# Optimization experiments

Measured on AMD Instinct MI355X. Metric: run time of the kernel, lower is better.

The kernel has to match this reference:

```python
import jax, jax.numpy as jnp
import numpy as np

W, B, C, H = 1600, 4, 1, 900
DENSITY = 0.03          # fraction of valid radar returns per column
DEPTH_MAX = 80.0        # metric depth range


def setup_inputs() -> dict:
    key = jax.random.key(0)
    k1, k2, k3 = jax.random.split(key, 3)
    radar_depth = jax.random.uniform(k1, (W, B, C, H, 1), jnp.float32) * DEPTH_MAX + 1.0
    radar_mask = jax.random.uniform(k2, (W, B, C, H, 1), jnp.float32) < DENSITY
    radar_patches = jnp.where(radar_mask, radar_depth, 0.0)
    # dense monocular depth estimate, strictly positive (all 'valid')
    mde_out_patches = jax.random.uniform(k3, (W, B, C, H, 1), jnp.float32) * DEPTH_MAX + 1.0
    return {"radar_patches": radar_patches, "mde_out_patches": mde_out_patches}


def _process_column(radar_col, mde_col):
    """Sequentially place valid radar depths of one (w,b) column.

    radar_col, mde_col: [H] float (channel 0 of the column).
    Returns radar_gt column [H].
    Matches torch loop: for each valid radar y (ascending), pick mde row with
    closest depth (argmin |mde - d|, first index on ties); if that slot is
    already occupied, search outward offsets +1,-1,+2,-2,... for an empty slot;
    if none found, overwrite the best slot.
    """
    h = radar_col.shape[0]
    ys = jnp.arange(h)
    mde_valid = mde_col != 0
    has_mde = jnp.any(mde_valid)
    BIG = jnp.float32(1e30)
    KBIG = 4 * h  # sentinel key for occupied slots

    def step(col, y):
        depth = radar_col[y]
        valid = depth != 0
        # per-point argmin over valid mde depths
        diffs = jnp.where(mde_valid, jnp.abs(mde_col - depth), BIG)
        best_y = jnp.where(has_mde, jnp.argmin(diffs), y)
        # outward collision search as a vectorized argmin over a priority key:
        #   best_y itself -> 0; offset o, +dy before -dy -> 2*o + (dy<0)
        occ = col != 0
        dy = ys - best_y
        key = 2 * jnp.abs(dy) + (dy < 0).astype(jnp.int32)
        key = jnp.where(ys == best_y, 0, key)
        key = jnp.where(occ, KBIG, key)
        final_y = jnp.argmin(key)
        # all slots occupied -> fall back to best_y (torch overwrites there)
        final_y = jnp.where(key[final_y] >= KBIG, best_y, final_y)
        new_col = jnp.where(valid, col.at[final_y].set(depth), col)
        return new_col, None

    col, _ = jax.lax.scan(step, jnp.zeros(h, radar_col.dtype), ys)
    return col


def reference(radar_patches, mde_out_patches):
    # channel 0 only is read/written, as in the torch code
    radar0 = radar_patches[:, :, 0, :, 0]   # [W, B, H]
    mde0 = mde_out_patches[:, :, 0, :, 0]   # [W, B, H]
    cols = jax.vmap(jax.vmap(_process_column))(radar0, mde0)  # [W, B, H]
    w, b, h = cols.shape
    c = radar_patches.shape[2]
    radar_gt = jnp.zeros((b, c, h, w), radar_patches.dtype)
    radar_gt = radar_gt.at[:, 0].set(jnp.transpose(cols, (1, 2, 0)))  # [B, H, W]
    return radar_gt
```

## Files before the change

### kernel.cpp

```cpp
#include <hip/hip_runtime.h>
#include <cstdint>
#include <cstddef>

#define WDIM 1600
#define BDIM 4
#define HDIM 900
#define NV4  225
#define QCAP 96
#define KBIG (4 * HDIM)
#define BW   6
#define NWAVE 4

#define DPP_MINF(v, ctrl)                                                  \
    v = fminf(v, __int_as_float(__builtin_amdgcn_update_dpp(               \
            __float_as_int(v), __float_as_int(v), ctrl, 0xf, 0xf, false)))

#define WAVE_FENCE() asm volatile("s_waitcnt lgkmcnt(0)" ::: "memory")

__global__ __launch_bounds__(256, 4) void radar_place_kernel(
    const float* __restrict__ radar, const float* __restrict__ mde,
    float* __restrict__ colout , int direct, float* __restrict__ out)
{
    __shared__ __align__(16) float s_col_all[NWAVE][HDIM];
    __shared__ float s_qd_all[NWAVE][QCAP];
    __shared__ int   s_qy_all[NWAVE][QCAP];

    const int lane = threadIdx.x & 63;
    const int wv   = threadIdx.x >> 6;
    const int colid = blockIdx.x * NWAVE + wv;

    float* s_col = s_col_all[wv];
    float* s_qd  = s_qd_all[wv];
    int*   s_qy  = s_qy_all[wv];

    const float4* mde4   = (const float4*)mde   + (long)colid * NV4;
    const float4* radar4 = (const float4*)radar + (long)colid * NV4;
    float4* col4 = (float4*)s_col;

    const unsigned long long below = (1ull << lane) - 1ull;

    bool hm = false;
#pragma unroll
    for (int c = 0; c < 4; ++c) {
        int i4 = c * 64 + lane;
        if (i4 < NV4) {
            float4 mv = mde4[i4];
            hm = hm || (mv.x != 0.f) || (mv.y != 0.f) || (mv.z != 0.f) || (mv.w != 0.f);
            col4[i4] = mv;
        }
    }
    const bool has_mde = (__ballot(hm) != 0ull);

    int Q = 0;
#pragma unroll
    for (int c = 0; c < 4; ++c) {
        int i4 = c * 64 + lane;
        bool in = (i4 < NV4);
        float4 rv = in ? radar4[i4] : make_float4(0.f, 0.f, 0.f, 0.f);
        unsigned long long b0 = __ballot(rv.x != 0.f);
        unsigned long long b1 = __ballot(rv.y != 0.f);
        unsigned long long b2 = __ballot(rv.z != 0.f);
        unsigned long long b3 = __ballot(rv.w != 0.f);
        int pos = Q + __popcll(b0 & below) + __popcll(b1 & below)
                    + __popcll(b2 & below) + __popcll(b3 & below);
        int y0 = i4 * 4;
        if (rv.x != 0.f) { if (pos < QCAP) { s_qd[pos] = rv.x; s_qy[pos] = y0;     } pos++; }
        if (rv.y != 0.f) { if (pos < QCAP) { s_qd[pos] = rv.y; s_qy[pos] = y0 + 1; } pos++; }
        if (rv.z != 0.f) { if (pos < QCAP) { s_qd[pos] = rv.z; s_qy[pos] = y0 + 2; } pos++; }
        if (rv.w != 0.f) { if (pos < QCAP) { s_qd[pos] = rv.w; s_qy[pos] = y0 + 3; } pos++; }
        Q += __popcll(b0) + __popcll(b1) + __popcll(b2) + __popcll(b3);
    }
    if (Q > QCAP) Q = QCAP;

    WAVE_FENCE();

    float m[15];
    if (lane < 60) {
        int yb = lane * 15;
#pragma unroll
        for (int k = 0; k < 15; ++k) {
            float v = s_col[yb + k];
            m[k] = (v != 0.f) ? v : 1e30f;
        }
    } else {
#pragma unroll
        for (int k = 0; k < 15; ++k) m[k] = 1e30f;
    }

    WAVE_FENCE();

#pragma unroll
    for (int c = 0; c < 4; ++c) {
        int i4 = c * 64 + lane;
        if (i4 < NV4) col4[i4] = make_float4(0.f, 0.f, 0.f, 0.f);
    }

    unsigned occ = (lane >= 60) ? 0x7FFFu : 0u;

    for (int t = 0; t < Q; t += BW) {
        float d[BW];
#pragma unroll
        for (int i = 0; i < BW; ++i) {
            int idx = (t + i < Q) ? (t + i) : (Q - 1);
            d[i] = s_qd[idx];
        }
        float bd[BW], bo[BW];
        int bik[BW];
#pragma unroll
        for (int i = 0; i < BW; ++i) { bd[i] = 3.4e38f; bik[i] = 0; }
#pragma unroll
        for (int k = 0; k < 15; ++k) {
            float mm = m[k];
#pragma unroll
            for (int i = 0; i < BW; ++i) {
                float af = fabsf(mm - d[i]);
                if (af < bd[i]) { bd[i] = af; bik[i] = k; }
            }
        }
#pragma unroll
        for (int i = 0; i < BW; ++i) bo[i] = bd[i];
#pragma unroll
        for (int i = 0; i < BW; ++i) DPP_MINF(bd[i], 0x111);
#pragma unroll
        for (int i = 0; i < BW; ++i) DPP_MINF(bd[i], 0x112);
#pragma unroll
        for (int i = 0; i < BW; ++i) DPP_MINF(bd[i], 0x114);
#pragma unroll
        for (int i = 0; i < BW; ++i) DPP_MINF(bd[i], 0x118);
#pragma unroll
        for (int i = 0; i < BW; ++i) DPP_MINF(bd[i], 0x142);
#pragma unroll
        for (int i = 0; i < BW; ++i) DPP_MINF(bd[i], 0x143);

#pragma unroll
        for (int i = 0; i < BW; ++i) {
            if (t + i < Q) {
                int best;
                if (has_mde) {
                    float gm = __int_as_float(
                        __builtin_amdgcn_readlane(__float_as_int(bd[i]), 63));
                    unsigned long long wm = __ballot(bo[i] == gm);
                    int win = __ffsll((long long)wm) - 1;
                    int kst = __shfl(bik[i], win);
                    best = win * 15 + kst;
                } else {
                    best = s_qy[t + i];
                }
                float depth = d[i];
                int sb = __builtin_amdgcn_readfirstlane(best);
                int bl = sb / 15, bk = sb % 15;
                unsigned long long bm = __ballot((occ >> bk) & 1u);
                int final_y = sb;
                if ((bm >> bl) & 1ull) {
                    int ko = 0x7fffffff, kk = 0;
#pragma unroll
                    for (int k = 0; k < 15; ++k) {
                        int yy = lane * 15 + k;
                        int o = (occ >> k) & 1;
                        int dy = yy - sb;
                        int ad = dy < 0 ? -dy : dy;
                        int key = o ? KBIG : (2 * ad + (dy < 0 ? 1 : 0));
                        if (key < ko) { ko = key; kk = k; }
                    }
                    int kmin = ko;
#pragma unroll
                    for (int off = 32; off; off >>= 1) {
                        int v = __shfl_xor(kmin, off);
                        kmin = (v < kmin) ? v : kmin;
                    }
                    if (kmin < KBIG) {
                        unsigned long long wm2 = __ballot(ko == kmin);
                        int w2 = __ffsll((long long)wm2) - 1;
                        int k2 = __shfl(kk, w2);
                        final_y = w2 * 15 + k2;
                    }
                }
                int sf = __builtin_amdgcn_readfirstlane(final_y);
                int fl = sf / 15, fk = sf % 15;
                if (lane == fl) occ |= (1u << fk);
                if (lane == 0) s_col[sf] = depth;
            }
        }
    }

    WAVE_FENCE();

    if (direct) {
        int w_ = colid >> 2, b_ = colid & 3;
#pragma unroll
        for (int c = 0; c < 4; ++c) {
            int i4 = c * 64 + lane;
            if (i4 < NV4) {
                float4 v = col4[i4];
                int y = i4 * 4;
                out[((long)(b_ * HDIM + y + 0)) * WDIM + w_] = v.x;
                out[((long)(b_ * HDIM + y + 1)) * WDIM + w_] = v.y;
                out[((long)(b_ * HDIM + y + 2)) * WDIM + w_] = v.z;
                out[((long)(b_ * HDIM + y + 3)) * WDIM + w_] = v.w;
            }
        }
    } else {
        float4* colout4 = (float4*)colout + (long)colid * NV4;
#pragma unroll
        for (int c = 0; c < 4; ++c) {
            int i4 = c * 64 + lane;
            if (i4 < NV4) colout4[i4] = col4[i4];
        }
    }
}

__global__ __launch_bounds__(256) void transpose_kernel(
    const float* __restrict__ colout, float* __restrict__ out)
{
    __shared__ float tile[32][33];
    const int b  = blockIdx.z;
    const int h0 = blockIdx.x * 32;
    const int w0 = blockIdx.y * 32;
    const int tx = threadIdx.x & 31;
    const int ty = threadIdx.x >> 5;
#pragma unroll
    for (int j = 0; j < 4; ++j) {
        int wl = ty + j * 8;
        int w = w0 + wl;
        int h = h0 + tx;
        float v = 0.0f;
        if (h < HDIM && w < WDIM) v = colout[((long)(w * BDIM + b)) * HDIM + h];
        tile[wl][tx] = v;
    }
    __syncthreads();
#pragma unroll
    for (int j = 0; j < 4; ++j) {
        int hl = ty + j * 8;
        int h = h0 + hl;
        int w = w0 + tx;
        if (h < HDIM && w < WDIM)
            out[((long)(b * HDIM + h)) * WDIM + w] = tile[tx][hl];
    }
}

extern "C" void kernel_launch(void* const* d_in, const int* in_sizes, int n_in,
                              void* d_out, int out_size, void* d_ws, size_t ws_size,
                              hipStream_t stream) {
    const float* radar = (const float*)d_in[0];
    const float* mde   = (const float*)d_in[1];
    float* out = (float*)d_out;
    float* ws  = (float*)d_ws;

    const size_t need = (size_t)WDIM * BDIM * HDIM * sizeof(float);
    const int direct = (ws_size < need) ? 1 : 0;

    hipLaunchKernelGGL(radar_place_kernel,
                       dim3(WDIM * BDIM / NWAVE), dim3(64 * NWAVE), 0, stream,
                       radar, mde, ws, direct, out);

    if (!direct) {
        dim3 g((HDIM + 31) / 32, WDIM / 32, BDIM);
        hipLaunchKernelGGL(transpose_kernel, g, dim3(256), 0, stream, ws, out);
    }
}
```

Measured before the change: 137.3 us.

## Split argmin pass from serial placement and decode collision slot from key

The per-point nearest-depth argmin now runs as a separate batched phase that writes each best row into the shared queue, with the batch width raised from 6 to 8. The serial placement loop then only resolves collisions. Queue entries are read into registers and broadcast with readlane, and the winning slot is recovered directly from the minimum priority key, so the second ballot and shuffle are gone. The integer min reduction uses DPP instead of xor shuffles. The intent is to shorten the serial dependency chain per radar point, at the cost of an extra pass and more register use.

```diff
diff --git a/kernel.cpp b/kernel.cpp
--- a/kernel.cpp
+++ b/kernel.cpp
@@ -8,12 +8,16 @@
 #define NV4  225
 #define QCAP 96
 #define KBIG (4 * HDIM)
-#define BW   6
+#define BW   8
 #define NWAVE 4
 
 #define DPP_MINF(v, ctrl)                                                  \
     v = fminf(v, __int_as_float(__builtin_amdgcn_update_dpp(               \
             __float_as_int(v), __float_as_int(v), ctrl, 0xf, 0xf, false)))
+
+#define DPP_MINI(v, ctrl)                                                  \
+    { int _dt = __builtin_amdgcn_update_dpp(v, v, ctrl, 0xf, 0xf, false);  \
+      v = (_dt < v) ? _dt : v; }
 
 #define WAVE_FENCE() asm volatile("s_waitcnt lgkmcnt(0)" ::: "memory")
 
@@ -95,92 +99,106 @@
         if (i4 < NV4) col4[i4] = make_float4(0.f, 0.f, 0.f, 0.f);
     }
 
+    if (has_mde) {
+        for (int t = 0; t < Q; t += BW) {
+            float d[BW];
+#pragma unroll
+            for (int i = 0; i < BW; ++i) {
+                int idx = (t + i < Q) ? (t + i) : (Q - 1);
+                d[i] = s_qd[idx];
+            }
+            float bd[BW], bo[BW];
+            int bik[BW];
+#pragma unroll
+            for (int i = 0; i < BW; ++i) { bd[i] = 3.4e38f; bik[i] = 0; }
+#pragma unroll
+            for (int k = 0; k < 15; ++k) {
+                float mm = m[k];
+#pragma unroll
+                for (int i = 0; i < BW; ++i) {
+                    float af = fabsf(mm - d[i]);
+                    if (af < bd[i]) { bd[i] = af; bik[i] = k; }
+                }
+            }
+#pragma unroll
+            for (int i = 0; i < BW; ++i) bo[i] = bd[i];
+#pragma unroll
+            for (int i = 0; i < BW; ++i) DPP_MINF(bd[i], 0x111);
+#pragma unroll
+            for (int i = 0; i < BW; ++i) DPP_MINF(bd[i], 0x112);
+#pragma unroll
+            for (int i = 0; i < BW; ++i) DPP_MINF(bd[i], 0x114);
+#pragma unroll
+            for (int i = 0; i < BW; ++i) DPP_MINF(bd[i], 0x118);
+#pragma unroll
+            for (int i = 0; i < BW; ++i) DPP_MINF(bd[i], 0x142);
+#pragma unroll
+            for (int i = 0; i < BW; ++i) DPP_MINF(bd[i], 0x143);
+
+#pragma unroll
+            for (int i = 0; i < BW; ++i) {
+                float gm = __int_as_float(
+                    __builtin_amdgcn_readlane(__float_as_int(bd[i]), 63));
+                unsigned long long wm = __ballot(bo[i] == gm);
+                int win = __ffsll((long long)wm) - 1;
+                int yall = lane * 15 + bik[i];
+                int sy = __builtin_amdgcn_readlane(yall, win);
+                if (lane == 0) s_qy[t + i] = sy;
+            }
+        }
+    }
+
+    WAVE_FENCE();
+
+    const int hi_idx = (64 + lane < QCAP) ? (64 + lane) : (QCAP - 1);
+    int   by0 = s_qy[lane];
+    int   by1 = s_qy[hi_idx];
+    float dp0 = s_qd[lane];
+    float dp1 = s_qd[hi_idx];
+
     unsigned occ = (lane >= 60) ? 0x7FFFu : 0u;
 
-    for (int t = 0; t < Q; t += BW) {
-        float d[BW];
-#pragma unroll
-        for (int i = 0; i < BW; ++i) {
-            int idx = (t + i < Q) ? (t + i) : (Q - 1);
-            d[i] = s_qd[idx];
-        }
-        float bd[BW], bo[BW];
-        int bik[BW];
-#pragma unroll
-        for (int i = 0; i < BW; ++i) { bd[i] = 3.4e38f; bik[i] = 0; }
-#pragma unroll
-        for (int k = 0; k < 15; ++k) {
-            float mm = m[k];
-#pragma unroll
-            for (int i = 0; i < BW; ++i) {
-                float af = fabsf(mm - d[i]);
-                if (af < bd[i]) { bd[i] = af; bik[i] = k; }
-            }
-        }
-#pragma unroll
-        for (int i = 0; i < BW; ++i) bo[i] = bd[i];
-#pragma unroll
-        for (int i = 0; i < BW; ++i) DPP_MINF(bd[i], 0x111);
-#pragma unroll
-        for (int i = 0; i < BW; ++i) DPP_MINF(bd[i], 0x112);
-#pragma unroll
-        for (int i = 0; i < BW; ++i) DPP_MINF(bd[i], 0x114);
-#pragma unroll
-        for (int i = 0; i < BW; ++i) DPP_MINF(bd[i], 0x118);
-#pragma unroll
-        for (int i = 0; i < BW; ++i) DPP_MINF(bd[i], 0x142);
-#pragma unroll
-        for (int i = 0; i < BW; ++i) DPP_MINF(bd[i], 0x143);
-
-#pragma unroll
-        for (int i = 0; i < BW; ++i) {
-            if (t + i < Q) {
-                int best;
-                if (has_mde) {
-                    float gm = __int_as_float(
-                        __builtin_amdgcn_readlane(__float_as_int(bd[i]), 63));
-                    unsigned long long wm = __ballot(bo[i] == gm);
-                    int win = __ffsll((long long)wm) - 1;
-                    int kst = __shfl(bik[i], win);
-                    best = win * 15 + kst;
-                } else {
-                    best = s_qy[t + i];
-                }
-                float depth = d[i];
-                int sb = __builtin_amdgcn_readfirstlane(best);
-                int bl = sb / 15, bk = sb % 15;
-                unsigned long long bm = __ballot((occ >> bk) & 1u);
-                int final_y = sb;
-                if ((bm >> bl) & 1ull) {
-                    int ko = 0x7fffffff, kk = 0;
-#pragma unroll
-                    for (int k = 0; k < 15; ++k) {
-                        int yy = lane * 15 + k;
-                        int o = (occ >> k) & 1;
-                        int dy = yy - sb;
-                        int ad = dy < 0 ? -dy : dy;
-                        int key = o ? KBIG : (2 * ad + (dy < 0 ? 1 : 0));
-                        if (key < ko) { ko = key; kk = k; }
-                    }
-                    int kmin = ko;
-#pragma unroll
-                    for (int off = 32; off; off >>= 1) {
-                        int v = __shfl_xor(kmin, off);
-                        kmin = (v < kmin) ? v : kmin;
-                    }
-                    if (kmin < KBIG) {
-                        unsigned long long wm2 = __ballot(ko == kmin);
-                        int w2 = __ffsll((long long)wm2) - 1;
-                        int k2 = __shfl(kk, w2);
-                        final_y = w2 * 15 + k2;
-                    }
-                }
-                int sf = __builtin_amdgcn_readfirstlane(final_y);
-                int fl = sf / 15, fk = sf % 15;
-                if (lane == fl) occ |= (1u << fk);
-                if (lane == 0) s_col[sf] = depth;
-            }
-        }
+    auto place = [&](int sb, float depth) {
+        int bl = sb / 15, bk = sb % 15;
+        unsigned ob = (unsigned)__builtin_amdgcn_readlane((int)occ, bl);
+        int fy = sb;
+        if ((ob >> bk) & 1u) {
+            int ko = 0x7fffffff;
+#pragma unroll
+            for (int k = 0; k < 15; ++k) {
+                int yy = lane * 15 + k;
+                int o = (occ >> k) & 1;
+                int dy = yy - sb;
+                int ad = dy < 0 ? -dy : dy;
+                int key = 2 * ad + (dy < 0 ? 1 : 0);
+                int pk = o ? 0x7fffffff : key;
+                ko = (pk < ko) ? pk : ko;
+            }
+            DPP_MINI(ko, 0x111);
+            DPP_MINI(ko, 0x112);
+            DPP_MINI(ko, 0x114);
+            DPP_MINI(ko, 0x118);
+            DPP_MINI(ko, 0x142);
+            DPP_MINI(ko, 0x143);
+            int kmin = __builtin_amdgcn_readlane(ko, 63);
+            if (kmin < KBIG)
+                fy = sb + ((kmin & 1) ? -(kmin >> 1) : (kmin >> 1));
+        }
+        int fl = fy / 15, fk = fy % 15;
+        occ |= (lane == fl) ? (1u << fk) : 0u;
+        if (lane == 0) s_col[fy] = depth;
+    };
+
+    const int qe = (Q < 64) ? Q : 64;
+    for (int q = 0; q < qe; ++q) {
+        int sb = __builtin_amdgcn_readlane(by0, q);
+        float dv = __int_as_float(__builtin_amdgcn_readlane(__float_as_int(dp0), q));
+        place(sb, dv);
+    }
+    for (int q = 64; q < Q; ++q) {
+        int sb = __builtin_amdgcn_readlane(by1, q - 64);
+        float dv = __int_as_float(__builtin_amdgcn_readlane(__float_as_int(dp1), q - 64));
+        place(sb, dv);
     }
 
     WAVE_FENCE();
```

Measured after the change: 148.4 us. +8.1%, slower.
